# Optimization experiments

Hardware: AMD Instinct MI355X
Metric: run time of the kernel (lower is better)

The kernel has to match this reference:

```python
import jax, jax.numpy as jnp
import numpy as np

# Conv3dOptimized: (depth-unfold via one-hot Conv2d) + 1x1 pointwise conv == standard
# Conv3d(C_in, C_out, k=3, padding=1) on BCHWD input, then BatchNorm (batch stats,
# training mode) per out-channel over (B,H,W,D), then LeakyReLU(0.2).

B, C_IN, C_OUT = 2, 32, 64
H, W, D = 96, 96, 35
K, PAD = 3, 1
NEG_SLOPE = 0.2
EPS = 1e-5


def setup_inputs() -> dict:
    key = jax.random.key(0)
    k1, k2, k3 = jax.random.split(key, 3)
    x = jax.random.normal(k1, (B, C_IN, H, W, D), dtype=jnp.float32)
    # Equivalent Conv3d weight (O, I, kH, kW, kD) -- composition of the one-hot
    # unfold conv and the learned pointwise conv weight.
    w = jax.random.normal(k2, (C_OUT, C_IN, K, K, K), dtype=jnp.float32) * 0.05
    b = jax.random.normal(k3, (C_OUT,), dtype=jnp.float32) * 0.05
    gamma = jnp.ones((C_OUT,), dtype=jnp.float32)   # BatchNorm affine init
    beta = jnp.zeros((C_OUT,), dtype=jnp.float32)
    return {"x": x, "w": w, "b": b, "gamma": gamma, "beta": beta}


def reference(x, w, b, gamma, beta):
    # x: (B, C_in, H, W, D); spatial dims are H, W, D.
    dn = jax.lax.conv_dimension_numbers(x.shape, w.shape, ("NCHWD", "OIHWD", "NCHWD"))
    out = jax.lax.conv_general_dilated(
        x, w, window_strides=(1, 1, 1), padding=[(PAD, PAD)] * 3,
        dimension_numbers=dn)
    out = out + b[None, :, None, None, None]
    # BatchNorm2d (training mode): batch stats per channel over (B, H, W*D)
    # == per channel over (B, H, W, D); biased variance, eps=1e-5.
    mean = jnp.mean(out, axis=(0, 2, 3, 4), keepdims=True)
    var = jnp.mean(jnp.square(out - mean), axis=(0, 2, 3, 4), keepdims=True)
    out = (out - mean) * jax.lax.rsqrt(var + EPS)
    out = out * gamma[None, :, None, None, None] + beta[None, :, None, None, None]
    # LeakyReLU(negative_slope=0.2)
    return jnp.where(out >= 0, out, NEG_SLOPE * out)
```

## Files before the change

### kernel.cpp

```cpp
#include <hip/hip_runtime.h>

#define B_    2
#define CI_   32
#define CO_   64
#define H_    96
#define W_    96
#define D_    35
#define PLANE (H_ * W_ * D_)
#define NPC   (B_ * PLANE)
#define HWD_  (H_ * W_ * D_)

constexpr int TW  = 6;
constexpr int PD  = 37;
constexpr int RP  = 300;
constexpr int NFRAG = 14;
constexpr float NEG = 0.2f;

typedef __attribute__((ext_vector_type(8))) short bf16x8;
typedef __attribute__((ext_vector_type(4))) float f32x4;

__device__ __forceinline__ unsigned short f2bf(float f) {
    unsigned u = __float_as_uint(f);
    u = (u + 0x7FFFu + ((u >> 16) & 1u)) >> 16;
    return (unsigned short)u;
}
__device__ __forceinline__ float bf2f(unsigned short h) {
    return __uint_as_float(((unsigned)h) << 16);
}

__global__ void zero_stats(float* stats) {
    if (threadIdx.x < 2 * CO_) stats[threadIdx.x] = 0.0f;
}

__global__ void prep_w(const float* __restrict__ wg, short* __restrict__ Bg) {
    int idx = blockIdx.x * 256 + threadIdx.x;
    if (idx < 27 * CO_ * CI_) {
        int tap = idx >> 11;
        int r   = idx & 2047;
        int co  = r >> 5, ci = r & 31;
        float v = wg[(co * CI_ + ci) * 27 + tap];
        unsigned short hi = f2bf(v);
        unsigned short lo = f2bf(v - bf2f(hi));
        Bg[tap * 2048 + r]              = (short)hi;
        Bg[27 * 2048 + tap * 2048 + r]  = (short)lo;
    }
}

__global__ __launch_bounds__(256, 2)
void conv_mfma_kernel(const float* __restrict__ x,
                      const short* __restrict__ Bg,
                      float* __restrict__ out,
                      float* __restrict__ stats) {
    __shared__ short As[3 * RP * 32];
    __shared__ short Bs[2][2][CO_ * 32];

    const int b   = blockIdx.z;
    const int h   = blockIdx.y;
    const int w0  = blockIdx.x * TW;
    const int tid = threadIdx.x;

    for (int u = tid; u < 3 * RP * 4; u += 256) {
        const int kh  = u / (RP * 4);
        const int r2  = u - kh * (RP * 4);
        const int mr  = r2 >> 2;
        const int oct = r2 & 3;
        const int wp  = mr / PD;
        const int dp  = mr - wp * PD;
        const int gh  = h + kh - 1;
        const int gw  = w0 + wp - 1;
        const int gd  = dp - 1;
        const bool vld = ((unsigned)gh < 96u) && (wp < 8) &&
                         ((unsigned)gw < 96u) && ((unsigned)gd < 35u);
        unsigned short h8[8];
        if (vld) {
            const float* xp = x + ((((size_t)b * CI_) * H_ + gh) * W_ + gw) * D_ + gd;
            #pragma unroll
            for (int j = 0; j < 8; ++j)
                h8[j] = f2bf(xp[(size_t)(oct * 8 + j) * HWD_]);
        } else {
            #pragma unroll
            for (int j = 0; j < 8; ++j) h8[j] = 0;
        }
        bf16x8 pk;
        #pragma unroll
        for (int j = 0; j < 8; ++j) pk[j] = (short)h8[j];
        *reinterpret_cast<bf16x8*>(&As[(kh * RP + mr) * 32 + oct * 8]) = pk;
    }

    const uint4* bg = reinterpret_cast<const uint4*>(Bg);
    {
        uint4 bh = bg[tid];
        uint4 bl = bg[6912 + tid];
        reinterpret_cast<uint4*>(&Bs[0][0][0])[tid] = bh;
        reinterpret_cast<uint4*>(&Bs[0][1][0])[tid] = bl;
    }
    __syncthreads();

    const int wave = tid >> 6;
    const int ln   = tid & 15;
    const int hk   = (tid >> 4) & 3;

    f32x4 acc[4][4] = {};

    for (int t = 0; t < 27; ++t) {
        const int buf = t & 1;
        uint4 nh = {}, nl = {};
        if (t + 1 < 27) {
            nh = bg[(t + 1) * 256 + tid];
            nl = bg[6912 + (t + 1) * 256 + tid];
        }
        const int kh = t / 9;
        const int kw = (t / 3) % 3;
        const int kd = t % 3;
        const int shift = (kw - 1) * PD + (kd - 1);

        bf16x8 Bf[4][2];
        #pragma unroll
        for (int n = 0; n < 4; ++n)
            #pragma unroll
            for (int v = 0; v < 2; ++v)
                Bf[n][v] = *reinterpret_cast<const bf16x8*>(
                    &Bs[buf][v][(n * 16 + ln) * 32 + hk * 8]);

        #pragma unroll
        for (int s = 0; s < 4; ++s) {
            const int fi = wave + 4 * s;
            if (fi < NFRAG) {
                const int row = kh * RP + 38 + 16 * fi + shift + ln;
                bf16x8 Af = *reinterpret_cast<const bf16x8*>(&As[row * 32 + hk * 8]);
                #pragma unroll
                for (int n = 0; n < 4; ++n) {
                    acc[s][n] = __builtin_amdgcn_mfma_f32_16x16x32_bf16(Af, Bf[n][0], acc[s][n], 0, 0, 0);
                    acc[s][n] = __builtin_amdgcn_mfma_f32_16x16x32_bf16(Af, Bf[n][1], acc[s][n], 0, 0, 0);
                }
            }
        }

        if (t + 1 < 27) {
            reinterpret_cast<uint4*>(&Bs[buf ^ 1][0][0])[tid] = nh;
            reinterpret_cast<uint4*>(&Bs[buf ^ 1][1][0])[tid] = nl;
        }
        __syncthreads();
    }

    float s1[4] = {0.f, 0.f, 0.f, 0.f};
    float s2[4] = {0.f, 0.f, 0.f, 0.f};
    #pragma unroll
    for (int s = 0; s < 4; ++s) {
        const int fi = wave + 4 * s;
        if (fi < NFRAG) {
            const int m0 = 38 + 16 * fi;
            #pragma unroll
            for (int r = 0; r < 4; ++r) {
                const int m  = m0 + hk * 4 + r;
                const int wp = m / PD;
                const int dp = m - wp * PD;
                if (dp >= 1 && dp <= 35 && wp >= 1 && wp <= TW) {
                    const int gw = w0 + wp - 1;
                    const int gd = dp - 1;
                    #pragma unroll
                    for (int n = 0; n < 4; ++n) {
                        const int co = n * 16 + ln;
                        const float vv = acc[s][n][r];
                        out[((((size_t)b * CO_ + co) * H_ + h) * W_ + gw) * D_ + gd] = vv;
                        s1[n] += vv;
                        s2[n] += vv * vv;
                    }
                }
            }
        }
    }
    #pragma unroll
    for (int n = 0; n < 4; ++n) {
        s1[n] += __shfl_xor(s1[n], 16);
        s1[n] += __shfl_xor(s1[n], 32);
        s2[n] += __shfl_xor(s2[n], 16);
        s2[n] += __shfl_xor(s2[n], 32);
    }
    if ((tid & 63) < 16) {
        #pragma unroll
        for (int n = 0; n < 4; ++n) {
            const int co = n * 16 + ln;
            atomicAdd(&stats[co * 2],     s1[n]);
            atomicAdd(&stats[co * 2 + 1], s2[n]);
        }
    }
}

__global__ void finalize_stats(const float* __restrict__ stats,
                               const float* __restrict__ gamma,
                               const float* __restrict__ beta,
                               float* __restrict__ ss) {
    const int c = threadIdx.x;
    if (c < CO_) {
        const float inv = 1.0f / (float)NPC;
        const float mean = stats[c * 2] * inv;
        const float var  = fmaf(-mean, mean, stats[c * 2 + 1] * inv);
        const float scale = gamma[c] * rsqrtf(var + 1e-5f);
        const float shift = fmaf(-mean, scale, beta[c]);
        ss[c * 2]     = scale;
        ss[c * 2 + 1] = shift;
    }
}

__global__ __launch_bounds__(256)
void bn_lrelu_kernel(float* __restrict__ out, const float* __restrict__ ss) {
    __shared__ float s_ss[CO_ * 2];
    if (threadIdx.x < CO_ * 2) s_ss[threadIdx.x] = ss[threadIdx.x];
    __syncthreads();
    constexpr int N4 = (B_ * CO_ * PLANE) / 4;
    constexpr int P4 = PLANE / 4;
    const int stride = gridDim.x * blockDim.x;
    for (int i = blockIdx.x * blockDim.x + threadIdx.x; i < N4; i += stride) {
        float4 v = reinterpret_cast<float4*>(out)[i];
        const int c = (i / P4) & (CO_ - 1);
        const float sc = s_ss[c * 2], sh = s_ss[c * 2 + 1];
        v.x = fmaf(v.x, sc, sh);
        v.y = fmaf(v.y, sc, sh);
        v.z = fmaf(v.z, sc, sh);
        v.w = fmaf(v.w, sc, sh);
        v.x = v.x >= 0.0f ? v.x : NEG * v.x;
        v.y = v.y >= 0.0f ? v.y : NEG * v.y;
        v.z = v.z >= 0.0f ? v.z : NEG * v.z;
        v.w = v.w >= 0.0f ? v.w : NEG * v.w;
        reinterpret_cast<float4*>(out)[i] = v;
    }
}

extern "C" void kernel_launch(void* const* d_in, const int* in_sizes, int n_in,
                              void* d_out, int out_size, void* d_ws, size_t ws_size,
                              hipStream_t stream) {
    const float* x     = (const float*)d_in[0];
    const float* wg    = (const float*)d_in[1];
    const float* gamma = (const float*)d_in[3];
    const float* beta  = (const float*)d_in[4];
    float* out   = (float*)d_out;

    char*  ws    = (char*)d_ws;
    float* stats = (float*)ws;
    float* ss    = (float*)(ws + 512);
    short* Bg    = (short*)(ws + 1024);

    zero_stats<<<1, 128, 0, stream>>>(stats);
    prep_w<<<(27 * CO_ * CI_ + 255) / 256, 256, 0, stream>>>(wg, Bg);

    dim3 grid(W_ / TW, H_, B_);
    conv_mfma_kernel<<<grid, 256, 0, stream>>>(x, Bg, out, stats);

    finalize_stats<<<1, 64, 0, stream>>>(stats, gamma, beta, ss);
    bn_lrelu_kernel<<<2048, 256, 0, stream>>>(out, ss);
}
```

Before: 875.6 us.

## Load conv weights straight to registers and drop per-tap LDS staging and barriers

The conv kernel no longer stages weight tiles through double-buffered shared memory with a __syncthreads per tap. Each lane now reads its B fragments directly from global memory (L2-resident) into ping-pong register sets, prefetching the next tap while the current one runs. The hi/lo weight layout is interleaved per tap, and the A tile in LDS is re-laid out by octet-major planes. The BN/LeakyReLU kernel becomes a 2D grid with per-block channel scale/shift, which removes the per-element division. In exchange, weight fragments are fetched redundantly by every block and register pressure rises.

```diff
diff --git a/kernel.cpp b/kernel.cpp
--- a/kernel.cpp
+++ b/kernel.cpp
@@ -41,8 +41,8 @@
         float v = wg[(co * CI_ + ci) * 27 + tap];
         unsigned short hi = f2bf(v);
         unsigned short lo = f2bf(v - bf2f(hi));
-        Bg[tap * 2048 + r]              = (short)hi;
-        Bg[27 * 2048 + tap * 2048 + r]  = (short)lo;
+        Bg[(tap * 2 + 0) * 2048 + r] = (short)hi;
+        Bg[(tap * 2 + 1) * 2048 + r] = (short)lo;
     }
 }
 
@@ -51,19 +51,18 @@
                       const short* __restrict__ Bg,
                       float* __restrict__ out,
                       float* __restrict__ stats) {
-    __shared__ short As[3 * RP * 32];
-    __shared__ short Bs[2][2][CO_ * 32];
+    __shared__ short As[3 * 4 * RP * 8];
 
     const int b   = blockIdx.z;
     const int h   = blockIdx.y;
     const int w0  = blockIdx.x * TW;
     const int tid = threadIdx.x;
 
-    for (int u = tid; u < 3 * RP * 4; u += 256) {
-        const int kh  = u / (RP * 4);
-        const int r2  = u - kh * (RP * 4);
-        const int mr  = r2 >> 2;
-        const int oct = r2 & 3;
+    for (int u = tid; u < 3 * 4 * RP; u += 256) {
+        const int kh  = u / (4 * RP);
+        const int r2  = u - kh * (4 * RP);
+        const int oct = r2 / RP;
+        const int mr  = r2 - oct * RP;
         const int wp  = mr / PD;
         const int dp  = mr - wp * PD;
         const int gh  = h + kh - 1;
@@ -71,77 +70,67 @@
         const int gd  = dp - 1;
         const bool vld = ((unsigned)gh < 96u) && (wp < 8) &&
                          ((unsigned)gw < 96u) && ((unsigned)gd < 35u);
-        unsigned short h8[8];
+        bf16x8 pk;
         if (vld) {
             const float* xp = x + ((((size_t)b * CI_) * H_ + gh) * W_ + gw) * D_ + gd;
             #pragma unroll
             for (int j = 0; j < 8; ++j)
-                h8[j] = f2bf(xp[(size_t)(oct * 8 + j) * HWD_]);
+                pk[j] = (short)f2bf(xp[(size_t)(oct * 8 + j) * HWD_]);
         } else {
             #pragma unroll
-            for (int j = 0; j < 8; ++j) h8[j] = 0;
-        }
-        bf16x8 pk;
-        #pragma unroll
-        for (int j = 0; j < 8; ++j) pk[j] = (short)h8[j];
-        *reinterpret_cast<bf16x8*>(&As[(kh * RP + mr) * 32 + oct * 8]) = pk;
-    }
-
-    const uint4* bg = reinterpret_cast<const uint4*>(Bg);
-    {
-        uint4 bh = bg[tid];
-        uint4 bl = bg[6912 + tid];
-        reinterpret_cast<uint4*>(&Bs[0][0][0])[tid] = bh;
-        reinterpret_cast<uint4*>(&Bs[0][1][0])[tid] = bl;
+            for (int j = 0; j < 8; ++j) pk[j] = 0;
+        }
+        *reinterpret_cast<bf16x8*>(&As[u * 8]) = pk;
     }
     __syncthreads();
 
     const int wave = tid >> 6;
     const int ln   = tid & 15;
     const int hk   = (tid >> 4) & 3;
+    const int pl   = ln * 32 + hk * 8;
 
     f32x4 acc[4][4] = {};
 
-    for (int t = 0; t < 27; ++t) {
-        const int buf = t & 1;
-        uint4 nh = {}, nl = {};
-        if (t + 1 < 27) {
-            nh = bg[(t + 1) * 256 + tid];
-            nl = bg[6912 + (t + 1) * 256 + tid];
+    bf16x8 bA[4][2], bB[4][2];
+    #pragma unroll
+    for (int n = 0; n < 4; ++n)
+        #pragma unroll
+        for (int v = 0; v < 2; ++v)
+            bA[n][v] = *reinterpret_cast<const bf16x8*>(Bg + v * 2048 + n * 512 + pl);
+
+    auto body = [&](int t, bf16x8 (&cur)[4][2], bf16x8 (&nxt)[4][2]) {
+        if (t < 26) {
+            const short* bp = Bg + (t + 1) * 4096 + pl;
+            #pragma unroll
+            for (int n = 0; n < 4; ++n)
+                #pragma unroll
+                for (int v = 0; v < 2; ++v)
+                    nxt[n][v] = *reinterpret_cast<const bf16x8*>(bp + v * 2048 + n * 512);
         }
         const int kh = t / 9;
         const int kw = (t / 3) % 3;
-        const int kd = t % 3;
+        const int kd = t - kh * 9 - kw * 3;
         const int shift = (kw - 1) * PD + (kd - 1);
-
-        bf16x8 Bf[4][2];
-        #pragma unroll
-        for (int n = 0; n < 4; ++n)
-            #pragma unroll
-            for (int v = 0; v < 2; ++v)
-                Bf[n][v] = *reinterpret_cast<const bf16x8*>(
-                    &Bs[buf][v][(n * 16 + ln) * 32 + hk * 8]);
-
+        const int cbase = (kh * 4 + hk) * RP + 38 + shift + ln;
         #pragma unroll
         for (int s = 0; s < 4; ++s) {
             const int fi = wave + 4 * s;
             if (fi < NFRAG) {
-                const int row = kh * RP + 38 + 16 * fi + shift + ln;
-                bf16x8 Af = *reinterpret_cast<const bf16x8*>(&As[row * 32 + hk * 8]);
+                bf16x8 Af = *reinterpret_cast<const bf16x8*>(&As[(cbase + 16 * fi) * 8]);
                 #pragma unroll
                 for (int n = 0; n < 4; ++n) {
-                    acc[s][n] = __builtin_amdgcn_mfma_f32_16x16x32_bf16(Af, Bf[n][0], acc[s][n], 0, 0, 0);
-                    acc[s][n] = __builtin_amdgcn_mfma_f32_16x16x32_bf16(Af, Bf[n][1], acc[s][n], 0, 0, 0);
+                    acc[s][n] = __builtin_amdgcn_mfma_f32_16x16x32_bf16(Af, cur[n][0], acc[s][n], 0, 0, 0);
+                    acc[s][n] = __builtin_amdgcn_mfma_f32_16x16x32_bf16(Af, cur[n][1], acc[s][n], 0, 0, 0);
                 }
             }
         }
-
-        if (t + 1 < 27) {
-            reinterpret_cast<uint4*>(&Bs[buf ^ 1][0][0])[tid] = nh;
-            reinterpret_cast<uint4*>(&Bs[buf ^ 1][1][0])[tid] = nl;
-        }
-        __syncthreads();
-    }
+    };
+
+    for (int tp = 0; tp < 13; ++tp) {
+        body(2 * tp,     bA, bB);
+        body(2 * tp + 1, bB, bA);
+    }
+    body(26, bA, bB);
 
     float s1[4] = {0.f, 0.f, 0.f, 0.f};
     float s2[4] = {0.f, 0.f, 0.f, 0.f};
@@ -205,25 +194,26 @@
 
 __global__ __launch_bounds__(256)
 void bn_lrelu_kernel(float* __restrict__ out, const float* __restrict__ ss) {
-    __shared__ float s_ss[CO_ * 2];
-    if (threadIdx.x < CO_ * 2) s_ss[threadIdx.x] = ss[threadIdx.x];
-    __syncthreads();
-    constexpr int N4 = (B_ * CO_ * PLANE) / 4;
-    constexpr int P4 = PLANE / 4;
-    const int stride = gridDim.x * blockDim.x;
-    for (int i = blockIdx.x * blockDim.x + threadIdx.x; i < N4; i += stride) {
-        float4 v = reinterpret_cast<float4*>(out)[i];
-        const int c = (i / P4) & (CO_ - 1);
-        const float sc = s_ss[c * 2], sh = s_ss[c * 2 + 1];
-        v.x = fmaf(v.x, sc, sh);
-        v.y = fmaf(v.y, sc, sh);
-        v.z = fmaf(v.z, sc, sh);
-        v.w = fmaf(v.w, sc, sh);
-        v.x = v.x >= 0.0f ? v.x : NEG * v.x;
-        v.y = v.y >= 0.0f ? v.y : NEG * v.y;
-        v.z = v.z >= 0.0f ? v.z : NEG * v.z;
-        v.w = v.w >= 0.0f ? v.w : NEG * v.w;
-        reinterpret_cast<float4*>(out)[i] = v;
+    const int bc = blockIdx.y;
+    const int c  = bc & (CO_ - 1);
+    const float sc = ss[c * 2], sh = ss[c * 2 + 1];
+    float4* p = reinterpret_cast<float4*>(out + (size_t)bc * PLANE);
+    const int i0 = blockIdx.x * 1024 + threadIdx.x;
+    #pragma unroll
+    for (int k = 0; k < 4; ++k) {
+        const int i = i0 + k * 256;
+        if (i < PLANE / 4) {
+            float4 v = p[i];
+            v.x = fmaf(v.x, sc, sh);
+            v.y = fmaf(v.y, sc, sh);
+            v.z = fmaf(v.z, sc, sh);
+            v.w = fmaf(v.w, sc, sh);
+            v.x = v.x >= 0.0f ? v.x : NEG * v.x;
+            v.y = v.y >= 0.0f ? v.y : NEG * v.y;
+            v.z = v.z >= 0.0f ? v.z : NEG * v.z;
+            v.w = v.w >= 0.0f ? v.w : NEG * v.w;
+            p[i] = v;
+        }
     }
 }
 
@@ -248,5 +238,7 @@
     conv_mfma_kernel<<<grid, 256, 0, stream>>>(x, Bg, out, stats);
 
     finalize_stats<<<1, 64, 0, stream>>>(stats, gamma, beta, ss);
-    bn_lrelu_kernel<<<2048, 256, 0, stream>>>(out, ss);
-}
+
+    dim3 grid4((PLANE / 4 + 1023) / 1024, B_ * CO_);
+    bn_lrelu_kernel<<<grid4, 256, 0, stream>>>(out, ss);
+}
```

Measured after the change: 874.1 us. No clear change (-0.2%).
